# Kernel optimization log

Hardware: AMD Instinct MI355X
Metric: run time of the kernel (lower is better)

## Reference

```python
import jax, jax.numpy as jnp
import numpy as np

B, N, C, H = 8, 4096, 1024, 16
D = C // H  # head_dim = 64
EPS = 1e-12

def _l2norm(x):
    # F.normalize(x, p=2, dim=-1): x / max(||x||_2, eps)
    n = jnp.sqrt(jnp.sum(x * x, axis=-1, keepdims=True))
    return x / jnp.maximum(n, EPS)

def setup_inputs() -> dict:
    key = jax.random.key(0)
    ks = jax.random.split(key, 5)
    return {
        "x": jax.random.normal(ks[0], (B, N, C), dtype=jnp.float32),
        "qkv_w": jax.random.normal(ks[1], (C, 3 * C), dtype=jnp.float32) * 0.02,
        "qkv_b": jax.random.normal(ks[2], (3 * C,), dtype=jnp.float32) * 0.02,
        "proj_w": jax.random.normal(ks[3], (C, C), dtype=jnp.float32) * 0.02,
        "proj_b": jax.random.normal(ks[4], (C,), dtype=jnp.float32) * 0.02,
    }

def reference(x, qkv_w, qkv_b, proj_w, proj_b):
    b, n, c = x.shape
    qkv = (x @ qkv_w + qkv_b).reshape(b, n, 3, H, D)
    qkv = jnp.transpose(qkv, (2, 0, 3, 1, 4))  # [3,B,H,N,D]
    q, k, v = qkv[0], qkv[1], qkv[2]
    q = _l2norm(q)
    k = _l2norm(k)
    kv = jnp.einsum('bhnd,bhne->bhde', k, v)   # small [B,H,D,D] state
    out = jnp.einsum('bhnd,bhde->bhne', q, kv)  # [B,H,N,D]
    out = jnp.transpose(out, (0, 2, 1, 3)).reshape(b, n, c)
    return out @ proj_w + proj_b
```

## Files before the change

### kernel.cpp

```cpp
#include <hip/hip_runtime.h>
#include <stdint.h>

#define B_ 8
#define N_ 4096
#define C_ 1024
#define H_ 16
#define M_ (B_*N_)
#define BH_ (B_*H_)

typedef unsigned short u16;
typedef unsigned int   u32;
typedef __bf16 bf16x8 __attribute__((ext_vector_type(8)));
typedef float  f32x4  __attribute__((ext_vector_type(4)));

__device__ __forceinline__ u16 f2bf(float f) {
  union { float f; u32 u; } x; x.f = f;
  u32 r = x.u + 0x7fffu + ((x.u >> 16) & 1u);
  return (u16)(r >> 16);
}
__device__ __forceinline__ float bf2f(u16 b) {
  union { u32 u; float f; } x; x.u = ((u32)b) << 16;
  return x.f;
}
__device__ __forceinline__ void gload16(const void* g, void* l) {
  __builtin_amdgcn_global_load_lds(
      (const __attribute__((address_space(1))) void*)g,
      (__attribute__((address_space(3))) void*)l,
      16, 0, 0);
}
__device__ __forceinline__ void unpack8(uint4 r, float* f) {
  const u32 w[4] = {r.x, r.y, r.z, r.w};
#pragma unroll
  for (int i = 0; i < 4; ++i) {
    f[2*i]   = bf2f((u16)(w[i] & 0xffffu));
    f[2*i+1] = bf2f((u16)(w[i] >> 16));
  }
}
__device__ __forceinline__ uint4 pack8(const float* f) {
  uint4 r; u32* w = (u32*)&r;
#pragma unroll
  for (int i = 0; i < 4; ++i)
    w[i] = (u32)f2bf(f[2*i]) | ((u32)f2bf(f[2*i+1]) << 16);
  return r;
}

#define BAR   __builtin_amdgcn_s_barrier()
#define LGKM0 asm volatile("s_waitcnt lgkmcnt(0)" ::: "memory")

__global__ void cast_f32_bf16(const float* __restrict__ in, u16* __restrict__ out, int n4) {
  int i = blockIdx.x * blockDim.x + threadIdx.x;
  const int stride = gridDim.x * blockDim.x;
  for (; i < n4; i += stride) {
    float4 v = reinterpret_cast<const float4*>(in)[i];
    u32 lo = (u32)f2bf(v.x) | ((u32)f2bf(v.y) << 16);
    u32 hi = (u32)f2bf(v.z) | ((u32)f2bf(v.w) << 16);
    uint2 o; o.x = lo; o.y = hi;
    reinterpret_cast<uint2*>(out)[i] = o;
  }
}

__global__ void transpose_cast(const float* __restrict__ in, u16* __restrict__ out,
                               int R, int Cc) {
  __shared__ float t[32][33];
  const int bx = blockIdx.x * 32;
  const int by = blockIdx.y * 32;
  const int tx = threadIdx.x & 31;
  const int ty = threadIdx.x >> 5;
#pragma unroll
  for (int j = 0; j < 4; ++j) {
    const int r = by + ty + j * 8;
    t[ty + j * 8][tx] = in[(size_t)r * Cc + bx + tx];
  }
  __syncthreads();
#pragma unroll
  for (int j = 0; j < 4; ++j) {
    const int c = bx + ty + j * 8;
    out[(size_t)c * R + by + tx] = f2bf(t[tx][ty + j * 8]);
  }
}

template <int NC, bool OUT_BF16>
__global__ __launch_bounds__(512) void gemm256(const u16* __restrict__ A,
                                               const u16* __restrict__ Bt,
                                               const float* __restrict__ bias,
                                               void* __restrict__ outp,
                                               int K, int cpx) {
  __shared__ __align__(16) u16 As[2][256 * 64];
  __shared__ __align__(16) u16 Bs[2][256 * 64];
  const int tid  = threadIdx.x;
  const int lane = tid & 63;
  const int w    = tid >> 6;
  const int wm   = (w >> 2) & 1;
  const int wn   = w & 3;
  const int l15  = lane & 15;
  const int lk   = lane >> 4;

  const int bid = blockIdx.x;
  const int wg  = (bid & 7) * cpx + (bid >> 3);
  const size_t brow = (size_t)(wg & 127) * 256;
  const size_t bcol = (size_t)(wg >> 7) * 256;

  const int KTn = K >> 6;
  f32x4 acc[2][2][4][2] = {};

  auto stage = [&](const u16* __restrict__ src, size_t rowbase, int kt,
                   u16* lds_tile, int h) {
#pragma unroll
    for (int is = 0; is < 2; ++is) {
      const int lin   = is * 8192 + tid * 16;
      const int row   = lin >> 7;
      const int chunk = ((lin >> 4) & 7) ^ (row & 7);
      gload16(src + (rowbase + (size_t)(h * 128 + row)) * K + kt * 64 + chunk * 8,
              (char*)lds_tile + h * 16384 + lin);
    }
  };
  auto fragA = [&](const u16* tb, int mh, int mf, int kc) -> bf16x8 {
    const int row   = mh * 128 + wm * 64 + mf * 16 + l15;
    const int chunk = ((kc << 2) | lk) ^ (row & 7);
    return *reinterpret_cast<const bf16x8*>((const char*)tb + row * 128 + chunk * 16);
  };
  auto fragB = [&](const u16* tb, int nh, int nf, int kc) -> bf16x8 {
    const int row   = nh * 128 + wn * 32 + nf * 16 + l15;
    const int chunk = ((kc << 2) | lk) ^ (row & 7);
    return *reinterpret_cast<const bf16x8*>((const char*)tb + row * 128 + chunk * 16);
  };

#define MFMA16(AF, BF, MH, NH) do {                                            \
    BAR; LGKM0;                                                                \
    __builtin_amdgcn_s_setprio(1);                                             \
    _Pragma("unroll") for (int mf = 0; mf < 4; ++mf)                           \
      _Pragma("unroll") for (int nf = 0; nf < 2; ++nf)                         \
        _Pragma("unroll") for (int kc = 0; kc < 2; ++kc)                       \
          acc[MH][NH][mf][nf] = __builtin_amdgcn_mfma_f32_16x16x32_bf16(       \
              AF[mf][kc], BF[nf][kc], acc[MH][NH][mf][nf], 0, 0, 0);           \
    __builtin_amdgcn_s_setprio(0);                                             \
    BAR;                                                                       \
  } while (0)

  stage(A,  brow, 0, As[0], 0);
  stage(Bt, bcol, 0, Bs[0], 0);
  stage(Bt, bcol, 0, Bs[0], 1);
  stage(A,  brow, 0, As[0], 1);
  stage(A,  brow, 1, As[1], 0);
  stage(Bt, bcol, 1, Bs[1], 0);
  stage(Bt, bcol, 1, Bs[1], 1);
  asm volatile("s_waitcnt vmcnt(6)" ::: "memory");
  BAR;

  for (int tt = 0; tt < KTn; tt += 2) {
    const bool s2 = (tt + 2) < KTn;
    bf16x8 a0[4][2], a1[4][2], b0[2][2], b1[2][2];

#pragma unroll
    for (int mf = 0; mf < 4; ++mf)
#pragma unroll
      for (int kc = 0; kc < 2; ++kc) a0[mf][kc] = fragA(As[0], 0, mf, kc);
#pragma unroll
    for (int nf = 0; nf < 2; ++nf)
#pragma unroll
      for (int kc = 0; kc < 2; ++kc) b0[nf][kc] = fragB(Bs[0], 0, nf, kc);
    stage(A, brow, tt + 1, As[1], 1);
    asm volatile("s_waitcnt lgkmcnt(8)");
    MFMA16(a0, b0, 0, 0);

#pragma unroll
    for (int nf = 0; nf < 2; ++nf)
#pragma unroll
      for (int kc = 0; kc < 2; ++kc) b1[nf][kc] = fragB(Bs[0], 1, nf, kc);
    if (s2) stage(A, brow, tt + 2, As[0], 0);
    MFMA16(a0, b1, 0, 1);

#pragma unroll
    for (int mf = 0; mf < 4; ++mf)
#pragma unroll
      for (int kc = 0; kc < 2; ++kc) a1[mf][kc] = fragA(As[0], 1, mf, kc);
    if (s2) stage(Bt, bcol, tt + 2, Bs[0], 0);
    MFMA16(a1, b1, 1, 1);

    if (s2) {
      stage(Bt, bcol, tt + 2, Bs[0], 1);
      asm volatile("s_waitcnt vmcnt(6)" ::: "memory");
    } else {
      asm volatile("s_waitcnt vmcnt(0)" ::: "memory");
    }
    MFMA16(a1, b0, 1, 0);

#pragma unroll
    for (int mf = 0; mf < 4; ++mf)
#pragma unroll
      for (int kc = 0; kc < 2; ++kc) a0[mf][kc] = fragA(As[1], 0, mf, kc);
#pragma unroll
    for (int nf = 0; nf < 2; ++nf)
#pragma unroll
      for (int kc = 0; kc < 2; ++kc) b0[nf][kc] = fragB(Bs[1], 0, nf, kc);
    if (s2) stage(A, brow, tt + 2, As[0], 1);
    asm volatile("s_waitcnt lgkmcnt(8)");
    MFMA16(a0, b0, 0, 0);

#pragma unroll
    for (int nf = 0; nf < 2; ++nf)
#pragma unroll
      for (int kc = 0; kc < 2; ++kc) b1[nf][kc] = fragB(Bs[1], 1, nf, kc);
    if (s2) stage(A, brow, tt + 3, As[1], 0);
    MFMA16(a0, b1, 0, 1);

#pragma unroll
    for (int mf = 0; mf < 4; ++mf)
#pragma unroll
      for (int kc = 0; kc < 2; ++kc) a1[mf][kc] = fragA(As[1], 1, mf, kc);
    if (s2) stage(Bt, bcol, tt + 3, Bs[1], 0);
    MFMA16(a1, b1, 1, 1);

    if (s2) {
      stage(Bt, bcol, tt + 3, Bs[1], 1);
      asm volatile("s_waitcnt vmcnt(6)" ::: "memory");
    } else {
      asm volatile("s_waitcnt vmcnt(0)" ::: "memory");
    }
    MFMA16(a1, b0, 1, 0);
  }
#undef MFMA16

#pragma unroll
  for (int mh = 0; mh < 2; ++mh)
#pragma unroll
  for (int nh = 0; nh < 2; ++nh)
#pragma unroll
  for (int mf = 0; mf < 4; ++mf)
#pragma unroll
  for (int nf = 0; nf < 2; ++nf) {
    const size_t col = bcol + nh * 128 + wn * 32 + nf * 16 + l15;
    const float bv = bias[col];
    const size_t row0 = brow + mh * 128 + wm * 64 + mf * 16 + lk * 4;
#pragma unroll
    for (int r = 0; r < 4; ++r) {
      const float v = acc[mh][nh][mf][nf][r] + bv;
      if constexpr (OUT_BF16)
        ((u16*)outp)[(row0 + r) * NC + col] = f2bf(v);
      else
        ((float*)outp)[(row0 + r) * NC + col] = v;
    }
  }
}

__global__ void prep(const u16* __restrict__ qkv, u16* __restrict__ KT,
                     u16* __restrict__ VT, float* __restrict__ qsc) {
  const int bh = blockIdx.x, nt = blockIdx.y;
  const int b = bh >> 4, h = bh & 15;
  const int n0 = nt * 64;
  const int tid = threadIdx.x;
  __shared__ float tk[64 * 65];

#pragma unroll
  for (int it = 0; it < 2; ++it) {
    const int idx = it * 256 + tid;
    const int r = idx >> 3, c8 = idx & 7;
    const size_t addr = ((size_t)(b * N_ + n0 + r)) * 3072 + h * 64 + c8 * 8;
    uint4 raw = *reinterpret_cast<const uint4*>(qkv + addr);
    float f[8]; unpack8(raw, f);
    float ss = 0.f;
#pragma unroll
    for (int j = 0; j < 8; ++j) ss += f[j] * f[j];
    ss += __shfl_xor(ss, 1); ss += __shfl_xor(ss, 2); ss += __shfl_xor(ss, 4);
    if (c8 == 0)
      qsc[((size_t)(b * N_ + n0 + r)) * 16 + h] = 1.f / fmaxf(sqrtf(ss), 1e-12f);
  }

#pragma unroll
  for (int it = 0; it < 2; ++it) {
    const int idx = it * 256 + tid;
    const int r = idx >> 3, c8 = idx & 7;
    const size_t addr = ((size_t)(b * N_ + n0 + r)) * 3072 + 1024 + h * 64 + c8 * 8;
    uint4 raw = *reinterpret_cast<const uint4*>(qkv + addr);
    float f[8]; unpack8(raw, f);
    float ss = 0.f;
#pragma unroll
    for (int j = 0; j < 8; ++j) ss += f[j] * f[j];
    ss += __shfl_xor(ss, 1); ss += __shfl_xor(ss, 2); ss += __shfl_xor(ss, 4);
    const float sc = 1.f / fmaxf(sqrtf(ss), 1e-12f);
#pragma unroll
    for (int j = 0; j < 8; ++j) tk[r * 65 + c8 * 8 + j] = f[j] * sc;
  }
  __syncthreads();
  {
    const int d = tid >> 2, nq = tid & 3;
    float v[16];
#pragma unroll
    for (int j = 0; j < 16; ++j) v[j] = tk[(nq * 16 + j) * 65 + d];
    u16* dst = KT + ((size_t)(bh * 64 + d)) * 4096 + n0 + nq * 16;
    *reinterpret_cast<uint4*>(dst)     = pack8(v);
    *reinterpret_cast<uint4*>(dst + 8) = pack8(v + 8);
  }
  __syncthreads();

#pragma unroll
  for (int it = 0; it < 2; ++it) {
    const int idx = it * 256 + tid;
    const int r = idx >> 3, c8 = idx & 7;
    const size_t addr = ((size_t)(b * N_ + n0 + r)) * 3072 + 2048 + h * 64 + c8 * 8;
    uint4 raw = *reinterpret_cast<const uint4*>(qkv + addr);
    float f[8]; unpack8(raw, f);
#pragma unroll
    for (int j = 0; j < 8; ++j) tk[r * 65 + c8 * 8 + j] = f[j];
  }
  __syncthreads();
  {
    const int e = tid >> 2, nq = tid & 3;
    float v[16];
#pragma unroll
    for (int j = 0; j < 16; ++j) v[j] = tk[(nq * 16 + j) * 65 + e];
    u16* dst = VT + ((size_t)(bh * 64 + e)) * 4096 + n0 + nq * 16;
    *reinterpret_cast<uint4*>(dst)     = pack8(v);
    *reinterpret_cast<uint4*>(dst + 8) = pack8(v + 8);
  }
}

__global__ void kv_gemm(const u16* __restrict__ VT, const u16* __restrict__ KT,
                        float* __restrict__ part) {
  const int bh = blockIdx.x, sp = blockIdx.y;
  __shared__ __align__(16) u16 Vs[64 * 64];
  __shared__ __align__(16) u16 Ks[64 * 64];
  const int tid  = threadIdx.x;
  const int lane = tid & 63;
  const int w    = tid >> 6;
  const int wm   = w >> 1, wn = w & 1;
  const int l15  = lane & 15;
  const int lk   = lane >> 4;

  f32x4 acc[2][2] = {};

  for (int kt = 0; kt < 16; ++kt) {
    const size_t k0 = (size_t)sp * 1024 + kt * 64;
#pragma unroll
    for (int is = 0; is < 2; ++is) {
      const int lin   = is * 4096 + tid * 16;
      const int row   = lin >> 7;
      const int chunk = ((lin >> 4) & 7) ^ (row & 7);
      gload16(VT + ((size_t)(bh * 64 + row)) * 4096 + k0 + chunk * 8, (char*)Vs + lin);
      gload16(KT + ((size_t)(bh * 64 + row)) * 4096 + k0 + chunk * 8, (char*)Ks + lin);
    }
    __syncthreads();
    bf16x8 fa[2][2], fb[2][2];
#pragma unroll
    for (int mf = 0; mf < 2; ++mf)
#pragma unroll
      for (int kc = 0; kc < 2; ++kc) {
        const int row = wm * 32 + mf * 16 + l15;
        const int chunk = ((kc << 2) | lk) ^ (row & 7);
        fa[mf][kc] = *reinterpret_cast<const bf16x8*>((const char*)Vs + row * 128 + chunk * 16);
      }
#pragma unroll
    for (int nf = 0; nf < 2; ++nf)
#pragma unroll
      for (int kc = 0; kc < 2; ++kc) {
        const int row = wn * 32 + nf * 16 + l15;
        const int chunk = ((kc << 2) | lk) ^ (row & 7);
        fb[nf][kc] = *reinterpret_cast<const bf16x8*>((const char*)Ks + row * 128 + chunk * 16);
      }
#pragma unroll
    for (int mf = 0; mf < 2; ++mf)
#pragma unroll
      for (int nf = 0; nf < 2; ++nf)
#pragma unroll
        for (int kc = 0; kc < 2; ++kc)
          acc[mf][nf] = __builtin_amdgcn_mfma_f32_16x16x32_bf16(
              fa[mf][kc], fb[nf][kc], acc[mf][nf], 0, 0, 0);
    __syncthreads();
  }

  float* base = part + ((size_t)sp * BH_ + bh) * 4096;
#pragma unroll
  for (int mf = 0; mf < 2; ++mf)
#pragma unroll
    for (int nf = 0; nf < 2; ++nf)
#pragma unroll
      for (int r = 0; r < 4; ++r) {
        const int e = wm * 32 + mf * 16 + lk * 4 + r;
        const int d = wn * 32 + nf * 16 + l15;
        base[e * 64 + d] = acc[mf][nf][r];
      }
}

__global__ void kv_reduce4(const float* __restrict__ part, u16* __restrict__ kvT) {
  const int i4 = (blockIdx.x * 256 + threadIdx.x) * 4;
  float4 s = *reinterpret_cast<const float4*>(part + i4);
#pragma unroll
  for (int sp = 1; sp < 4; ++sp) {
    float4 p = *reinterpret_cast<const float4*>(part + (size_t)sp * 524288 + i4);
    s.x += p.x; s.y += p.y; s.z += p.z; s.w += p.w;
  }
  u32 lo = (u32)f2bf(s.x) | ((u32)f2bf(s.y) << 16);
  u32 hi = (u32)f2bf(s.z) | ((u32)f2bf(s.w) << 16);
  uint2 o; o.x = lo; o.y = hi;
  *reinterpret_cast<uint2*>(kvT + i4) = o;
}

__global__ void attn_gemm(const u16* __restrict__ qkv, const u16* __restrict__ kvT,
                          const float* __restrict__ qsc, u16* __restrict__ attn) {
  const int bh = blockIdx.x, nt = blockIdx.y;
  const int b = bh >> 4, h = bh & 15;
  const int n0 = nt * 128;
  __shared__ __align__(16) u16 Qs[128 * 64];
  __shared__ __align__(16) u16 Ks[64 * 64];
  const int tid  = threadIdx.x;
  const int lane = tid & 63;
  const int wm   = tid >> 6;
  const int l15  = lane & 15;
  const int lk   = lane >> 4;

#pragma unroll
  for (int is = 0; is < 4; ++is) {
    const int lin   = is * 4096 + tid * 16;
    const int row   = lin >> 7;
    const int chunk = ((lin >> 4) & 7) ^ (row & 7);
    gload16(qkv + ((size_t)(b * N_ + n0 + row)) * 3072 + h * 64 + chunk * 8,
            (char*)Qs + lin);
  }
#pragma unroll
  for (int is = 0; is < 2; ++is) {
    const int lin   = is * 4096 + tid * 16;
    const int row   = lin >> 7;
    const int chunk = ((lin >> 4) & 7) ^ (row & 7);
    gload16(kvT + (size_t)bh * 4096 + row * 64 + chunk * 8, (char*)Ks + lin);
  }
  __syncthreads();

  bf16x8 fq[2][2], fk[4][2];
#pragma unroll
  for (int mf = 0; mf < 2; ++mf)
#pragma unroll
    for (int kc = 0; kc < 2; ++kc) {
      const int row = wm * 32 + mf * 16 + l15;
      const int chunk = ((kc << 2) | lk) ^ (row & 7);
      fq[mf][kc] = *reinterpret_cast<const bf16x8*>((const char*)Qs + row * 128 + chunk * 16);
    }
#pragma unroll
  for (int nf = 0; nf < 4; ++nf)
#pragma unroll
    for (int kc = 0; kc < 2; ++kc) {
      const int row = nf * 16 + l15;
      const int chunk = ((kc << 2) | lk) ^ (row & 7);
      fk[nf][kc] = *reinterpret_cast<const bf16x8*>((const char*)Ks + row * 128 + chunk * 16);
    }
  f32x4 acc[2][4] = {};
#pragma unroll
  for (int mf = 0; mf < 2; ++mf)
#pragma unroll
    for (int nf = 0; nf < 4; ++nf)
#pragma unroll
      for (int kc = 0; kc < 2; ++kc)
        acc[mf][nf] = __builtin_amdgcn_mfma_f32_16x16x32_bf16(
            fq[mf][kc], fk[nf][kc], acc[mf][nf], 0, 0, 0);

#pragma unroll
  for (int mf = 0; mf < 2; ++mf)
#pragma unroll
    for (int r = 0; r < 4; ++r) {
      const size_t row = (size_t)(b * N_ + n0 + wm * 32 + mf * 16 + lk * 4 + r);
      const float sc = qsc[row * 16 + h];
#pragma unroll
      for (int nf = 0; nf < 4; ++nf)
        attn[row * 1024 + h * 64 + nf * 16 + l15] = f2bf(acc[mf][nf][r] * sc);
    }
}

#define WS_XB     0ull
#define WS_QKV    67108864ull
#define WS_VT     268435456ull
#define WS_WQKV   335544320ull
#define WS_WPROJ  341835776ull
#define WS_PART   343932928ull
#define WS_QSC    352321536ull
#define WS_KVT    360710144ull

extern "C" void kernel_launch(void* const* d_in, const int* in_sizes, int n_in,
                              void* d_out, int out_size, void* d_ws, size_t ws_size,
                              hipStream_t stream) {
  const float* x      = (const float*)d_in[0];
  const float* qkv_w  = (const float*)d_in[1];
  const float* qkv_b  = (const float*)d_in[2];
  const float* proj_w = (const float*)d_in[3];
  const float* proj_b = (const float*)d_in[4];

  char* ws = (char*)d_ws;
  u16*   xb      = (u16*)(ws + WS_XB);
  u16*   KT      = (u16*)(ws + WS_XB);
  u16*   qkv     = (u16*)(ws + WS_QKV);
  u16*   VT      = (u16*)(ws + WS_VT);
  u16*   attn    = (u16*)(ws + WS_VT);
  u16*   wqkv_t  = (u16*)(ws + WS_WQKV);
  u16*   wproj_t = (u16*)(ws + WS_WPROJ);
  float* part    = (float*)(ws + WS_PART);
  float* qsc     = (float*)(ws + WS_QSC);
  u16*   kvT     = (u16*)(ws + WS_KVT);

  cast_f32_bf16<<<2048, 256, 0, stream>>>(x, xb, (M_ * C_) / 4);
  transpose_cast<<<dim3(96, 32), 256, 0, stream>>>(qkv_w, wqkv_t, 1024, 3072);
  transpose_cast<<<dim3(32, 32), 256, 0, stream>>>(proj_w, wproj_t, 1024, 1024);
  gemm256<3072, true><<<1536, 512, 0, stream>>>(xb, wqkv_t, qkv_b, qkv, 1024, 192);
  prep<<<dim3(128, 64), 256, 0, stream>>>(qkv, KT, VT, qsc);
  kv_gemm<<<dim3(128, 4), 256, 0, stream>>>(VT, KT, part);
  kv_reduce4<<<512, 256, 0, stream>>>(part, kvT);
  attn_gemm<<<dim3(128, 32), 256, 0, stream>>>(qkv, kvT, qsc, attn);
  gemm256<1024, false><<<512, 512, 0, stream>>>(attn, wproj_t, proj_b, d_out, 1024, 64);
}
```

Baseline: 506.2 us.

## Use 4 waves per GEMM block with 128x128 warp tiles and prefetched fragments

```diff
diff --git a/kernel.cpp b/kernel.cpp
--- a/kernel.cpp
+++ b/kernel.cpp
@@ -44,8 +44,9 @@
   return r;
 }
 
-#define BAR   __builtin_amdgcn_s_barrier()
-#define LGKM0 asm volatile("s_waitcnt lgkmcnt(0)" ::: "memory")
+#define BAR       __builtin_amdgcn_s_barrier()
+#define LGKM(N)   asm volatile("s_waitcnt lgkmcnt(" #N ")" ::: "memory")
+#define VMCNT(N)  asm volatile("s_waitcnt vmcnt(" #N ")" ::: "memory")
 
 __global__ void cast_f32_bf16(const float* __restrict__ in, u16* __restrict__ out, int n4) {
   int i = blockIdx.x * blockDim.x + threadIdx.x;
@@ -80,18 +81,18 @@
 }
 
 template <int NC, bool OUT_BF16>
-__global__ __launch_bounds__(512) void gemm256(const u16* __restrict__ A,
-                                               const u16* __restrict__ Bt,
-                                               const float* __restrict__ bias,
-                                               void* __restrict__ outp,
-                                               int K, int cpx) {
+__global__ __launch_bounds__(256, 1) void gemm256(const u16* __restrict__ A,
+                                                  const u16* __restrict__ Bt,
+                                                  const float* __restrict__ bias,
+                                                  void* __restrict__ outp,
+                                                  int K, int cpx) {
   __shared__ __align__(16) u16 As[2][256 * 64];
   __shared__ __align__(16) u16 Bs[2][256 * 64];
   const int tid  = threadIdx.x;
   const int lane = tid & 63;
   const int w    = tid >> 6;
-  const int wm   = (w >> 2) & 1;
-  const int wn   = w & 3;
+  const int wm   = w >> 1;
+  const int wn   = w & 1;
   const int l15  = lane & 15;
   const int lk   = lane >> 4;
 
@@ -101,125 +102,121 @@
   const size_t bcol = (size_t)(wg >> 7) * 256;
 
   const int KTn = K >> 6;
-  f32x4 acc[2][2][4][2] = {};
+  f32x4 acc[2][2][4][4] = {};
 
   auto stage = [&](const u16* __restrict__ src, size_t rowbase, int kt,
                    u16* lds_tile, int h) {
 #pragma unroll
-    for (int is = 0; is < 2; ++is) {
-      const int lin   = is * 8192 + tid * 16;
+    for (int is = 0; is < 4; ++is) {
+      const int lin   = is * 4096 + tid * 16;
       const int row   = lin >> 7;
       const int chunk = ((lin >> 4) & 7) ^ (row & 7);
       gload16(src + (rowbase + (size_t)(h * 128 + row)) * K + kt * 64 + chunk * 8,
               (char*)lds_tile + h * 16384 + lin);
     }
   };
-  auto fragA = [&](const u16* tb, int mh, int mf, int kc) -> bf16x8 {
-    const int row   = mh * 128 + wm * 64 + mf * 16 + l15;
-    const int chunk = ((kc << 2) | lk) ^ (row & 7);
-    return *reinterpret_cast<const bf16x8*>((const char*)tb + row * 128 + chunk * 16);
+  auto readA = [&](bf16x8 (&d)[4][2], const u16* tb, int mh) {
+#pragma unroll
+    for (int mf = 0; mf < 4; ++mf)
+#pragma unroll
+      for (int kc = 0; kc < 2; ++kc) {
+        const int row   = mh * 128 + wm * 64 + mf * 16 + l15;
+        const int chunk = ((kc << 2) | lk) ^ (row & 7);
+        d[mf][kc] = *reinterpret_cast<const bf16x8*>((const char*)tb + row * 128 + chunk * 16);
+      }
   };
-  auto fragB = [&](const u16* tb, int nh, int nf, int kc) -> bf16x8 {
-    const int row   = nh * 128 + wn * 32 + nf * 16 + l15;
-    const int chunk = ((kc << 2) | lk) ^ (row & 7);
-    return *reinterpret_cast<const bf16x8*>((const char*)tb + row * 128 + chunk * 16);
+  auto readB = [&](bf16x8 (&d)[4][2], const u16* tb, int nh) {
+#pragma unroll
+    for (int nf = 0; nf < 4; ++nf)
+#pragma unroll
+      for (int kc = 0; kc < 2; ++kc) {
+        const int row   = nh * 128 + wn * 64 + nf * 16 + l15;
+        const int chunk = ((kc << 2) | lk) ^ (row & 7);
+        d[nf][kc] = *reinterpret_cast<const bf16x8*>((const char*)tb + row * 128 + chunk * 16);
+      }
   };
-
-#define MFMA16(AF, BF, MH, NH) do {                                            \
-    BAR; LGKM0;                                                                \
-    __builtin_amdgcn_s_setprio(1);                                             \
-    _Pragma("unroll") for (int mf = 0; mf < 4; ++mf)                           \
-      _Pragma("unroll") for (int nf = 0; nf < 2; ++nf)                         \
-        _Pragma("unroll") for (int kc = 0; kc < 2; ++kc)                       \
-          acc[MH][NH][mf][nf] = __builtin_amdgcn_mfma_f32_16x16x32_bf16(       \
-              AF[mf][kc], BF[nf][kc], acc[MH][NH][mf][nf], 0, 0, 0);           \
-    __builtin_amdgcn_s_setprio(0);                                             \
-    BAR;                                                                       \
-  } while (0)
+  auto quad = [&](bf16x8 (&af)[4][2], bf16x8 (&bf)[4][2], f32x4 (&ac)[4][4]) {
+    __builtin_amdgcn_s_setprio(1);
+#pragma unroll
+    for (int kc = 0; kc < 2; ++kc)
+#pragma unroll
+      for (int mf = 0; mf < 4; ++mf)
+#pragma unroll
+        for (int nf = 0; nf < 4; ++nf)
+          ac[mf][nf] = __builtin_amdgcn_mfma_f32_16x16x32_bf16(
+              af[mf][kc], bf[nf][kc], ac[mf][nf], 0, 0, 0);
+    __builtin_amdgcn_s_setprio(0);
+  };
+
+  bf16x8 a0[4][2], a1[4][2], b1[4][2], b0e[4][2], b0o[4][2];
 
   stage(A,  brow, 0, As[0], 0);
   stage(Bt, bcol, 0, Bs[0], 0);
+  stage(A,  brow, 0, As[0], 1);
   stage(Bt, bcol, 0, Bs[0], 1);
-  stage(A,  brow, 0, As[0], 1);
   stage(A,  brow, 1, As[1], 0);
   stage(Bt, bcol, 1, Bs[1], 0);
   stage(Bt, bcol, 1, Bs[1], 1);
-  asm volatile("s_waitcnt vmcnt(6)" ::: "memory");
+  VMCNT(12);
   BAR;
+  readA(a0, As[0], 0);
+  readB(b0e, Bs[0], 0);
 
   for (int tt = 0; tt < KTn; tt += 2) {
     const bool s2 = (tt + 2) < KTn;
-    bf16x8 a0[4][2], a1[4][2], b0[2][2], b1[2][2];
-
-#pragma unroll
-    for (int mf = 0; mf < 4; ++mf)
-#pragma unroll
-      for (int kc = 0; kc < 2; ++kc) a0[mf][kc] = fragA(As[0], 0, mf, kc);
-#pragma unroll
-    for (int nf = 0; nf < 2; ++nf)
-#pragma unroll
-      for (int kc = 0; kc < 2; ++kc) b0[nf][kc] = fragB(Bs[0], 0, nf, kc);
+
     stage(A, brow, tt + 1, As[1], 1);
-    asm volatile("s_waitcnt lgkmcnt(8)");
-    MFMA16(a0, b0, 0, 0);
-
-#pragma unroll
-    for (int nf = 0; nf < 2; ++nf)
-#pragma unroll
-      for (int kc = 0; kc < 2; ++kc) b1[nf][kc] = fragB(Bs[0], 1, nf, kc);
+    readB(b1, Bs[0], 1);
+    BAR; LGKM(8);
+    quad(a0, b0e, acc[0][0]);
+    BAR;
+
     if (s2) stage(A, brow, tt + 2, As[0], 0);
-    MFMA16(a0, b1, 0, 1);
-
-#pragma unroll
-    for (int mf = 0; mf < 4; ++mf)
-#pragma unroll
-      for (int kc = 0; kc < 2; ++kc) a1[mf][kc] = fragA(As[0], 1, mf, kc);
+    readA(a1, As[0], 1);
+    BAR; LGKM(8);
+    quad(a0, b1, acc[0][1]);
+    BAR;
+
     if (s2) stage(Bt, bcol, tt + 2, Bs[0], 0);
-    MFMA16(a1, b1, 1, 1);
-
-    if (s2) {
-      stage(Bt, bcol, tt + 2, Bs[0], 1);
-      asm volatile("s_waitcnt vmcnt(6)" ::: "memory");
-    } else {
-      asm volatile("s_waitcnt vmcnt(0)" ::: "memory");
-    }
-    MFMA16(a1, b0, 1, 0);
-
-#pragma unroll
-    for (int mf = 0; mf < 4; ++mf)
-#pragma unroll
-      for (int kc = 0; kc < 2; ++kc) a0[mf][kc] = fragA(As[1], 0, mf, kc);
-#pragma unroll
-    for (int nf = 0; nf < 2; ++nf)
-#pragma unroll
-      for (int kc = 0; kc < 2; ++kc) b0[nf][kc] = fragB(Bs[1], 0, nf, kc);
+    BAR; LGKM(0);
+    quad(a1, b1, acc[1][1]);
+    BAR;
+
+    if (s2) { stage(Bt, bcol, tt + 2, Bs[0], 1); VMCNT(12); }
+    else    { VMCNT(0); }
+    BAR;
+    readA(a0, As[1], 0);
+    readB(b0o, Bs[1], 0);
+    LGKM(15);
+    quad(a1, b0e, acc[1][0]);
+    BAR;
+
     if (s2) stage(A, brow, tt + 2, As[0], 1);
-    asm volatile("s_waitcnt lgkmcnt(8)");
-    MFMA16(a0, b0, 0, 0);
-
-#pragma unroll
-    for (int nf = 0; nf < 2; ++nf)
-#pragma unroll
-      for (int kc = 0; kc < 2; ++kc) b1[nf][kc] = fragB(Bs[1], 1, nf, kc);
+    readB(b1, Bs[1], 1);
+    BAR; LGKM(8);
+    quad(a0, b0o, acc[0][0]);
+    BAR;
+
     if (s2) stage(A, brow, tt + 3, As[1], 0);
-    MFMA16(a0, b1, 0, 1);
-
-#pragma unroll
-    for (int mf = 0; mf < 4; ++mf)
-#pragma unroll
-      for (int kc = 0; kc < 2; ++kc) a1[mf][kc] = fragA(As[1], 1, mf, kc);
+    readA(a1, As[1], 1);
+    BAR; LGKM(8);
+    quad(a0, b1, acc[0][1]);
+    BAR;
+
     if (s2) stage(Bt, bcol, tt + 3, Bs[1], 0);
-    MFMA16(a1, b1, 1, 1);
-
-    if (s2) {
-      stage(Bt, bcol, tt + 3, Bs[1], 1);
-      asm volatile("s_waitcnt vmcnt(6)" ::: "memory");
-    } else {
-      asm volatile("s_waitcnt vmcnt(0)" ::: "memory");
-    }
-    MFMA16(a1, b0, 1, 0);
-  }
-#undef MFMA16
+    BAR; LGKM(0);
+    quad(a1, b1, acc[1][1]);
+    BAR;
+
+    if (s2) { stage(Bt, bcol, tt + 3, Bs[1], 1); VMCNT(12); }
+    else    { VMCNT(0); }
+    BAR;
+    readA(a0, As[0], 0);
+    readB(b0e, Bs[0], 0);
+    LGKM(15);
+    quad(a1, b0o, acc[1][0]);
+    BAR;
+  }
 
 #pragma unroll
   for (int mh = 0; mh < 2; ++mh)
@@ -228,8 +225,8 @@
 #pragma unroll
   for (int mf = 0; mf < 4; ++mf)
 #pragma unroll
-  for (int nf = 0; nf < 2; ++nf) {
-    const size_t col = bcol + nh * 128 + wn * 32 + nf * 16 + l15;
+  for (int nf = 0; nf < 4; ++nf) {
+    const size_t col = bcol + nh * 128 + wn * 64 + nf * 16 + l15;
     const float bv = bias[col];
     const size_t row0 = brow + mh * 128 + wm * 64 + mf * 16 + lk * 4;
 #pragma unroll
@@ -497,10 +494,10 @@
   cast_f32_bf16<<<2048, 256, 0, stream>>>(x, xb, (M_ * C_) / 4);
   transpose_cast<<<dim3(96, 32), 256, 0, stream>>>(qkv_w, wqkv_t, 1024, 3072);
   transpose_cast<<<dim3(32, 32), 256, 0, stream>>>(proj_w, wproj_t, 1024, 1024);
-  gemm256<3072, true><<<1536, 512, 0, stream>>>(xb, wqkv_t, qkv_b, qkv, 1024, 192);
+  gemm256<3072, true><<<1536, 256, 0, stream>>>(xb, wqkv_t, qkv_b, qkv, 1024, 192);
   prep<<<dim3(128, 64), 256, 0, stream>>>(qkv, KT, VT, qsc);
   kv_gemm<<<dim3(128, 4), 256, 0, stream>>>(VT, KT, part);
   kv_reduce4<<<512, 256, 0, stream>>>(part, kvT);
   attn_gemm<<<dim3(128, 32), 256, 0, stream>>>(qkv, kvT, qsc, attn);
-  gemm256<1024, false><<<512, 512, 0, stream>>>(attn, wproj_t, proj_b, d_out, 1024, 64);
-}
+  gemm256<1024, false><<<512, 256, 0, stream>>>(attn, wproj_t, proj_b, d_out, 1024, 64);
+}
```

After: 1.206 ms. 2.38x slower.
